# Performance work log

Measured on AMD Instinct MI355X. Metric: run time of the kernel, lower is better.

The kernel has to match this reference:

```python
import jax, jax.numpy as jnp
import numpy as np

D = 384
H = 6
DK = D // H
EPS = 1e-5


def _layernorm(x, g, b):
    mu = jnp.mean(x, axis=-1, keepdims=True)
    var = jnp.var(x, axis=-1, keepdims=True)
    return (x - mu) * jax.lax.rsqrt(var + EPS) * g + b


def setup_inputs() -> dict:
    key = jax.random.key(0)
    ks = jax.random.split(key, 12)
    B, N = 8, 2048
    s = lambda fan_in: 1.0 / np.sqrt(fan_in)
    return {
        "points": jax.random.normal(ks[0], (B, 3 + D, N), dtype=jnp.float32),
        "ln1_g": jnp.ones((D,), jnp.float32),
        "ln1_b": jnp.zeros((D,), jnp.float32),
        "w_qkv": jax.random.uniform(ks[1], (3 * D, D), jnp.float32, -s(D), s(D)),
        "w_o": jax.random.uniform(ks[2], (D, D), jnp.float32, -s(D), s(D)),
        "b_o": jnp.zeros((D,), jnp.float32),
        "ln2_g": jnp.ones((D,), jnp.float32),
        "ln2_b": jnp.zeros((D,), jnp.float32),
        "w1": jax.random.uniform(ks[3], (2 * D, D), jnp.float32, -s(D), s(D)),
        "b1": jnp.zeros((2 * D,), jnp.float32),
        "w2": jax.random.uniform(ks[4], (D, 2 * D), jnp.float32, -s(2 * D), s(2 * D)),
        "b2": jnp.zeros((D,), jnp.float32),
    }


def reference(points, ln1_g, ln1_b, w_qkv, w_o, b_o, ln2_g, ln2_b, w1, b1, w2, b2):
    coords = points[:, :3, :]                       # [B, 3, N]
    feats = jnp.transpose(points[:, 3:, :], (0, 2, 1))  # [B, N, D]
    B, N, _ = feats.shape

    # pre-norm + fused QKV projection (no bias)
    h = _layernorm(feats, ln1_g, ln1_b)
    qkv = jnp.einsum('bnd,ed->bne', h, w_qkv)       # [B, N, 3D]
    q, k, v = jnp.split(qkv, 3, axis=-1)

    split_heads = lambda t: jnp.transpose(t.reshape(B, N, H, DK), (0, 2, 1, 3))
    q, k, v = split_heads(q), split_heads(k), split_heads(v)  # [B, H, N, DK]

    scale = DK ** -0.5
    scores = jnp.einsum('bhid,bhjd->bhij', q, k) * scale      # [B, H, N, N]
    attn = jax.nn.softmax(scores, axis=-1)
    ctx = jnp.einsum('bhij,bhjd->bhid', attn, v)              # [B, H, N, DK]
    ctx = jnp.transpose(ctx, (0, 2, 1, 3)).reshape(B, N, D)
    attn_out = jnp.einsum('bnd,ed->bne', ctx, w_o) + b_o

    x = feats + attn_out
    # FFN with exact (erf) GELU, hidden = 2*D
    h2 = _layernorm(x, ln2_g, ln2_b)
    ff = jnp.einsum('bnd,ed->bne', h2, w1) + b1
    ff = jax.nn.gelu(ff, approximate=False)
    ff = jnp.einsum('bne,de->bnd', ff, w2) + b2
    x = x + ff

    return jnp.concatenate([coords, jnp.transpose(x, (0, 2, 1))], axis=1)
```

## Files before the change

kernel.cpp:

```cpp
#include <hip/hip_runtime.h>
#include <cstdint>


typedef __bf16 bf16;
typedef __bf16 bf16x8 __attribute__((ext_vector_type(8)));
typedef __bf16 bf16x4 __attribute__((ext_vector_type(4)));
typedef short s16x4 __attribute__((ext_vector_type(4)));
typedef float floatx4 __attribute__((ext_vector_type(4)));
typedef uint32_t __attribute__((address_space(1))) gu32;
typedef uint32_t __attribute__((address_space(3))) lu32;

#define NN 2048
#define DD 384
#define HH 6
#define DK 64
#define BB 8
#define MM (BB * NN)
#define D3 (3 * DD)
#define D2 (2 * DD)
#define CH (3 + DD)
#define LP 72
#define LPV 136

#define QSCALE 0.18033688011112042f

static __device__ __forceinline__ s16x4 as_s16x4(bf16x4 v) {
    union { bf16x4 b; s16x4 s; } u; u.b = v; return u.s;
}


__global__ void cast_all_kernel(const float* __restrict__ w_qkv, const float* __restrict__ w_o,
                                const float* __restrict__ w1, const float* __restrict__ w2,
                                bf16* __restrict__ o_qkv, bf16* __restrict__ o_o,
                                bf16* __restrict__ o_w1, bf16* __restrict__ o_w2) {
    int i = blockIdx.x * 256 + threadIdx.x;
    if (i < 442368) o_qkv[i] = (bf16)w_qkv[i];
    else if (i < 589824) o_o[i - 442368] = (bf16)w_o[i - 442368];
    else if (i < 884736) o_w1[i - 589824] = (bf16)w1[i - 589824];
    else o_w2[i - 884736] = (bf16)w2[i - 884736];
}

__global__ void coords_kernel(const float* __restrict__ pts, float* __restrict__ out) {
    int i = blockIdx.x * 256 + threadIdx.x;
    int b = i / (3 * NN), r = i % (3 * NN);
    out[(size_t)b * CH * NN + r] = pts[(size_t)b * CH * NN + r];
}

__global__ void transpose_kernel(const float* __restrict__ pts, float* __restrict__ feats) {
    __shared__ float T[32][33];
    int n0 = blockIdx.x * 32, d0 = blockIdx.y * 32, b = blockIdx.z;
    int tx = threadIdx.x, ty = threadIdx.y;
    const float* src = pts + (size_t)b * CH * NN;
#pragma unroll
    for (int i = 0; i < 4; ++i)
        T[ty + i * 8][tx] = src[(size_t)(3 + d0 + ty + i * 8) * NN + n0 + tx];
    __syncthreads();
    float* dst = feats + (size_t)b * NN * DD;
#pragma unroll
    for (int i = 0; i < 4; ++i)
        dst[(size_t)(n0 + ty + i * 8) * DD + d0 + tx] = T[tx][ty + i * 8];
}

__global__ __launch_bounds__(256) void ln_kernel(const float* __restrict__ x,
                                                 const float* __restrict__ g,
                                                 const float* __restrict__ bta,
                                                 bf16* __restrict__ out) {
    int wave = threadIdx.x >> 6, lane = threadIdx.x & 63;
    int row = blockIdx.x * 4 + wave;
    const float* xr = x + (size_t)row * DD;
    float v[6], s = 0.f, sq = 0.f;
#pragma unroll
    for (int i = 0; i < 6; ++i) { v[i] = xr[lane + i * 64]; s += v[i]; sq += v[i] * v[i]; }
#pragma unroll
    for (int o = 1; o < 64; o <<= 1) { s += __shfl_xor(s, o); sq += __shfl_xor(sq, o); }
    float mu = s * (1.f / DD);
    float var = sq * (1.f / DD) - mu * mu;
    float rs = rsqrtf(var + 1e-5f);
    bf16* orow = out + (size_t)row * DD;
#pragma unroll
    for (int i = 0; i < 6; ++i) {
        int d = lane + i * 64;
        orow[d] = (bf16)((v[i] - mu) * rs * g[d] + bta[d]);
    }
}

template <int NC, int K, int MODE, int TN>
__global__ __launch_bounds__(256, 2)
void gemm_bt(const bf16* __restrict__ A, const bf16* __restrict__ W,
             const float* __restrict__ bias, const float* __restrict__ res,
             bf16* __restrict__ obf, float* __restrict__ of32, bf16* __restrict__ vt) {
    constexpr int MI = (TN == 128) ? 4 : 2;
    __shared__ bf16 As[128 * 32];
    __shared__ bf16 Ws[TN * 32];
    const int t = threadIdx.x;
    const int wave = t >> 6, lane = t & 63;
    const int m0 = blockIdx.x * 128, n0 = blockIdx.y * TN;
    const int wm = (TN == 128) ? (wave >> 1) * 64 : wave * 32;
    const int wn = (TN == 128) ? (wave & 1) * 64 : 0;
    const int lr = lane & 15, quad = lane >> 4;
    const int sr = t >> 2, sc = (t & 3) * 8;

    floatx4 acc[MI][4];
#pragma unroll
    for (int mi = 0; mi < MI; ++mi)
#pragma unroll
        for (int ni = 0; ni < 4; ++ni) {
            floatx4 z = {0.f, 0.f, 0.f, 0.f};
            acc[mi][ni] = z;
        }

    for (int k0 = 0; k0 < K; k0 += 32) {
        __syncthreads();
#pragma unroll
        for (int i = 0; i < 2; ++i) {
            const int r = i * 64 + sr;
            __builtin_amdgcn_global_load_lds(
                (const gu32*)&A[(size_t)(m0 + r) * K + k0 + sc],
                (lu32*)&As[r * 32 + sc], 16, 0, 0);
        }
#pragma unroll
        for (int i = 0; i < TN / 64; ++i) {
            const int r = i * 64 + sr;
            __builtin_amdgcn_global_load_lds(
                (const gu32*)&W[(size_t)(n0 + r) * K + k0 + sc],
                (lu32*)&Ws[r * 32 + sc], 16, 0, 0);
        }
        __syncthreads();
        bf16x8 af[MI], bfr[4];
#pragma unroll
        for (int mi = 0; mi < MI; ++mi)
            af[mi] = *(const bf16x8*)&As[(wm + mi * 16 + lr) * 32 + quad * 8];
#pragma unroll
        for (int ni = 0; ni < 4; ++ni)
            bfr[ni] = *(const bf16x8*)&Ws[(wn + ni * 16 + lr) * 32 + quad * 8];
#pragma unroll
        for (int mi = 0; mi < MI; ++mi)
#pragma unroll
            for (int ni = 0; ni < 4; ++ni)
                acc[mi][ni] = __builtin_amdgcn_mfma_f32_16x16x32_bf16(af[mi], bfr[ni], acc[mi][ni], 0, 0, 0);
    }

#pragma unroll
    for (int mi = 0; mi < MI; ++mi) {
#pragma unroll
        for (int ni = 0; ni < 4; ++ni) {
            const int r0 = m0 + wm + mi * 16 + quad * 4;
            const int c = n0 + wn + ni * 16 + lr;
            floatx4 v = acc[mi][ni];
            if constexpr (MODE == 0) {
                const int cb = n0 + wn + ni * 16;
                if (cb >= 2 * DD) {
                    const int hh = (c - 2 * DD) >> 6, dk = (c - 2 * DD) & 63;
                    const int b = r0 >> 11, n = r0 & (NN - 1);
                    bf16x4 pk;
#pragma unroll
                    for (int r = 0; r < 4; ++r) pk[r] = (bf16)v[r];
                    *(bf16x4*)&vt[((size_t)(b * HH + hh) * DK + dk) * NN + n] = pk;
                } else {
                    const float sc_q = (cb < DD) ? QSCALE : 1.0f;
#pragma unroll
                    for (int r = 0; r < 4; ++r) obf[(size_t)(r0 + r) * NC + c] = (bf16)(v[r] * sc_q);
                }
            } else if constexpr (MODE == 1) {
#pragma unroll
                for (int r = 0; r < 4; ++r)
                    of32[(size_t)(r0 + r) * NC + c] = v[r] + bias[c] + res[(size_t)(r0 + r) * NC + c];
            } else if constexpr (MODE == 2) {
#pragma unroll
                for (int r = 0; r < 4; ++r) {
                    float u = v[r] + bias[c];
                    obf[(size_t)(r0 + r) * NC + c] = (bf16)(0.5f * u * (1.f + erff(u * 0.70710678118f)));
                }
            } else {
                const int b = r0 >> 11, n = r0 & (NN - 1);
                float o4[4];
#pragma unroll
                for (int r = 0; r < 4; ++r)
                    o4[r] = v[r] + bias[c] + res[(size_t)(r0 + r) * DD + c];
                float4 val = make_float4(o4[0], o4[1], o4[2], o4[3]);
                *(float4*)&of32[((size_t)b * CH + 3 + c) * NN + n] = val;
            }
        }
    }
}

__global__ __launch_bounds__(256, 3)
void attn_kernel(const bf16* __restrict__ qkv, const bf16* __restrict__ vt,
                 bf16* __restrict__ ctx) {
    __shared__ bf16 Ks[128 * LP];
    __shared__ bf16 Vs[64 * LPV];
    const int t = threadIdx.x, wave = t >> 6, lane = t & 63;
    const int lr = lane & 15, quad = lane >> 4;
    const int bh = blockIdx.y, b = bh / HH, h = bh % HH;
    const int q0 = blockIdx.x * 128 + wave * 32;
    const bf16* qbase = qkv + (size_t)b * NN * D3 + h * DK;
    const bf16* kbase = qbase + DD;
    const bf16* vbase = vt + (size_t)bh * DK * NN;

    bf16x8 aq[2][2];
#pragma unroll
    for (int mi = 0; mi < 2; ++mi)
#pragma unroll
        for (int ks = 0; ks < 2; ++ks)
            aq[mi][ks] = *(const bf16x8*)&qbase[(size_t)(q0 + mi * 16 + lr) * D3 +
                                                ks * 32 + quad * 8];

    bf16x4 ones4;
#pragma unroll
    for (int i = 0; i < 4; ++i) ones4[i] = (bf16)1.0f;
    const s16x4 ones_s = as_s16x4(ones4);

    floatx4 o[2][4], ol[2];
#pragma unroll
    for (int mi = 0; mi < 2; ++mi) {
        floatx4 z = {0.f, 0.f, 0.f, 0.f};
        ol[mi] = z;
#pragma unroll
        for (int nd = 0; nd < 4; ++nd) o[mi][nd] = z;
    }

    for (int j0 = 0; j0 < NN; j0 += 128) {
        __syncthreads();
        {
            const int rr = t >> 3, cc = (t & 7) * 8;
#pragma unroll
            for (int i = 0; i < 4; ++i) {
                const int j = i * 32 + rr;
                *(bf16x8*)&Ks[j * LP + cc] =
                    *(const bf16x8*)&kbase[(size_t)(j0 + j) * D3 + cc];
            }
            const int rr2 = t >> 4, cc2 = (t & 15) * 8;
#pragma unroll
            for (int i = 0; i < 4; ++i) {
                const int d = i * 16 + rr2;
                *(bf16x8*)&Vs[d * LPV + cc2] =
                    *(const bf16x8*)&vbase[(size_t)d * NN + j0 + cc2];
            }
        }
        __syncthreads();

        floatx4 s[2][8];
#pragma unroll
        for (int mi = 0; mi < 2; ++mi)
#pragma unroll
            for (int nj = 0; nj < 8; ++nj) {
                floatx4 z = {0.f, 0.f, 0.f, 0.f};
                s[mi][nj] = z;
            }
#pragma unroll
        for (int ks = 0; ks < 2; ++ks)
#pragma unroll
            for (int nj = 0; nj < 8; ++nj) {
                bf16x8 bk = *(const bf16x8*)&Ks[(nj * 16 + lr) * LP + ks * 32 + quad * 8];
#pragma unroll
                for (int mi = 0; mi < 2; ++mi)
                    s[mi][nj] = __builtin_amdgcn_mfma_f32_16x16x32_bf16(bk, aq[mi][ks],
                                                                        s[mi][nj], 0, 0, 0);
            }

#pragma unroll
        for (int nj = 0; nj < 8; ++nj) {
            s16x4 ap[2];
#pragma unroll
            for (int mi = 0; mi < 2; ++mi) {
                bf16x4 pk;
#pragma unroll
                for (int r = 0; r < 4; ++r) pk[r] = (bf16)exp2f(s[mi][nj][r]);
                ap[mi] = as_s16x4(pk);
            }
#pragma unroll
            for (int nd = 0; nd < 4; ++nd) {
                s16x4 bv = as_s16x4(*(const bf16x4*)&Vs[(nd * 16 + lr) * LPV +
                                                        nj * 16 + quad * 4]);
#pragma unroll
                for (int mi = 0; mi < 2; ++mi)
                    o[mi][nd] = __builtin_amdgcn_mfma_f32_16x16x16bf16_1k(ap[mi], bv,
                                                                          o[mi][nd], 0, 0, 0);
            }
#pragma unroll
            for (int mi = 0; mi < 2; ++mi)
                ol[mi] = __builtin_amdgcn_mfma_f32_16x16x16bf16_1k(ap[mi], ones_s, ol[mi], 0, 0, 0);
        }
    }

#pragma unroll
    for (int mi = 0; mi < 2; ++mi)
#pragma unroll
        for (int r = 0; r < 4; ++r) {
            const int n = q0 + mi * 16 + quad * 4 + r;
            const float inv = 1.0f / ol[mi][r];
#pragma unroll
            for (int nd = 0; nd < 4; ++nd) {
                const int d = h * DK + nd * 16 + lr;
                ctx[(size_t)(b * NN + n) * DD + d] = (bf16)(o[mi][nd][r] * inv);
            }
        }
}


extern "C" void kernel_launch(void* const* d_in, const int* in_sizes, int n_in,
                              void* d_out, int out_size, void* d_ws, size_t ws_size,
                              hipStream_t stream) {
    const float* points = (const float*)d_in[0];
    const float* ln1_g = (const float*)d_in[1];
    const float* ln1_b = (const float*)d_in[2];
    const float* w_qkv = (const float*)d_in[3];
    const float* w_o   = (const float*)d_in[4];
    const float* b_o   = (const float*)d_in[5];
    const float* ln2_g = (const float*)d_in[6];
    const float* ln2_b = (const float*)d_in[7];
    const float* w1    = (const float*)d_in[8];
    const float* b1    = (const float*)d_in[9];
    const float* w2    = (const float*)d_in[10];
    const float* b2    = (const float*)d_in[11];
    float* out = (float*)d_out;

    char* ws = (char*)d_ws;
    size_t off = 0;
    auto alloc = [&](size_t bytes) -> void* {
        void* p = ws + off;
        off += (bytes + 255) & ~(size_t)255;
        return p;
    };
    float* feats = (float*)alloc((size_t)MM * DD * 4);
    float* xbuf  = (float*)alloc((size_t)MM * DD * 4);
    bf16* h1     = (bf16*)alloc((size_t)MM * DD * 2);
    bf16* h2     = (bf16*)alloc((size_t)MM * DD * 2);
    bf16* qkvb   = (bf16*)alloc((size_t)MM * D3 * 2);
    bf16* vtb    = (bf16*)alloc((size_t)BB * HH * DK * NN * 2);
    bf16* ctx    = (bf16*)alloc((size_t)MM * DD * 2);
    bf16* ffh    = (bf16*)alloc((size_t)MM * D2 * 2);
    bf16* wqkv_bf = (bf16*)alloc((size_t)D3 * DD * 2);
    bf16* wo_bf   = (bf16*)alloc((size_t)DD * DD * 2);
    bf16* w1_bf   = (bf16*)alloc((size_t)D2 * DD * 2);
    bf16* w2_bf   = (bf16*)alloc((size_t)DD * D2 * 2);

    cast_all_kernel<<<1179648 / 256, 256, 0, stream>>>(w_qkv, w_o, w1, w2,
                                                       wqkv_bf, wo_bf, w1_bf, w2_bf);
    coords_kernel<<<(BB * 3 * NN) / 256, 256, 0, stream>>>(points, out);
    transpose_kernel<<<dim3(NN / 32, DD / 32, BB), dim3(32, 8), 0, stream>>>(points, feats);
    ln_kernel<<<MM / 4, 256, 0, stream>>>(feats, ln1_g, ln1_b, h1);
    gemm_bt<D3, DD, 0, 128><<<dim3(MM / 128, D3 / 128), 256, 0, stream>>>(
        h1, wqkv_bf, nullptr, nullptr, qkvb, nullptr, vtb);
    attn_kernel<<<dim3(NN / 128, BB * HH), 256, 0, stream>>>(qkvb, vtb, ctx);
    gemm_bt<DD, DD, 1, 64><<<dim3(MM / 128, DD / 64), 256, 0, stream>>>(
        ctx, wo_bf, b_o, feats, nullptr, xbuf, nullptr);
    ln_kernel<<<MM / 4, 256, 0, stream>>>(xbuf, ln2_g, ln2_b, h2);
    gemm_bt<D2, DD, 2, 128><<<dim3(MM / 128, D2 / 128), 256, 0, stream>>>(
        h2, w1_bf, b1, nullptr, ffh, nullptr, nullptr);
    gemm_bt<DD, D2, 3, 64><<<dim3(MM / 128, DD / 64), 256, 0, stream>>>(
        ffh, w2_bf, b2, xbuf, nullptr, out, nullptr);
}
```

Before: 290.5 us.

## Prefetch next K/V tile into registers and raise wave priority around MFMA blocks

The attention kernel now loads the next 128-key K and V tiles from global memory into registers while the current tile is being computed, then writes them to shared memory at the top of the next iteration. This hides global load latency behind the QK and PV MFMA work. It also wraps the MFMA sections in s_setprio so waves issuing matrix ops get scheduling priority. The cost is 8 extra vector registers per thread, which may pressure occupancy at launch bounds of 3 blocks.

```diff
diff --git a/kernel.cpp b/kernel.cpp
--- a/kernel.cpp
+++ b/kernel.cpp
@@ -197,6 +197,9 @@
     const bf16* kbase = qbase + DD;
     const bf16* vbase = vt + (size_t)bh * DK * NN;
 
+    const int rr = t >> 3, cc = (t & 7) * 8;
+    const int rr2 = t >> 4, cc2 = (t & 15) * 8;
+
     bf16x8 aq[2][2];
 #pragma unroll
     for (int mi = 0; mi < 2; ++mi)
@@ -219,23 +222,30 @@
         for (int nd = 0; nd < 4; ++nd) o[mi][nd] = z;
     }
 
+    bf16x8 pk[4], pv[4];
+#pragma unroll
+    for (int i = 0; i < 4; ++i)
+        pk[i] = *(const bf16x8*)&kbase[(size_t)(i * 32 + rr) * D3 + cc];
+#pragma unroll
+    for (int i = 0; i < 4; ++i)
+        pv[i] = *(const bf16x8*)&vbase[(size_t)(i * 16 + rr2) * NN + cc2];
+
     for (int j0 = 0; j0 < NN; j0 += 128) {
         __syncthreads();
-        {
-            const int rr = t >> 3, cc = (t & 7) * 8;
-#pragma unroll
-            for (int i = 0; i < 4; ++i) {
-                const int j = i * 32 + rr;
-                *(bf16x8*)&Ks[j * LP + cc] =
-                    *(const bf16x8*)&kbase[(size_t)(j0 + j) * D3 + cc];
-            }
-            const int rr2 = t >> 4, cc2 = (t & 15) * 8;
-#pragma unroll
-            for (int i = 0; i < 4; ++i) {
-                const int d = i * 16 + rr2;
-                *(bf16x8*)&Vs[d * LPV + cc2] =
-                    *(const bf16x8*)&vbase[(size_t)d * NN + j0 + cc2];
-            }
+#pragma unroll
+        for (int i = 0; i < 4; ++i)
+            *(bf16x8*)&Ks[(i * 32 + rr) * LP + cc] = pk[i];
+#pragma unroll
+        for (int i = 0; i < 4; ++i)
+            *(bf16x8*)&Vs[(i * 16 + rr2) * LPV + cc2] = pv[i];
+        if (j0 + 128 < NN) {
+            const int jn = j0 + 128;
+#pragma unroll
+            for (int i = 0; i < 4; ++i)
+                pk[i] = *(const bf16x8*)&kbase[(size_t)(jn + i * 32 + rr) * D3 + cc];
+#pragma unroll
+            for (int i = 0; i < 4; ++i)
+                pv[i] = *(const bf16x8*)&vbase[(size_t)(i * 16 + rr2) * NN + jn + cc2];
         }
         __syncthreads();
 
@@ -247,6 +257,7 @@
                 floatx4 z = {0.f, 0.f, 0.f, 0.f};
                 s[mi][nj] = z;
             }
+        __builtin_amdgcn_s_setprio(1);
 #pragma unroll
         for (int ks = 0; ks < 2; ++ks)
 #pragma unroll
@@ -257,17 +268,19 @@
                     s[mi][nj] = __builtin_amdgcn_mfma_f32_16x16x32_bf16(bk, aq[mi][ks],
                                                                         s[mi][nj], 0, 0, 0);
             }
+        __builtin_amdgcn_s_setprio(0);
 
 #pragma unroll
         for (int nj = 0; nj < 8; ++nj) {
             s16x4 ap[2];
 #pragma unroll
             for (int mi = 0; mi < 2; ++mi) {
-                bf16x4 pk;
-#pragma unroll
-                for (int r = 0; r < 4; ++r) pk[r] = (bf16)exp2f(s[mi][nj][r]);
-                ap[mi] = as_s16x4(pk);
-            }
+                bf16x4 pk4;
+#pragma unroll
+                for (int r = 0; r < 4; ++r) pk4[r] = (bf16)exp2f(s[mi][nj][r]);
+                ap[mi] = as_s16x4(pk4);
+            }
+            __builtin_amdgcn_s_setprio(1);
 #pragma unroll
             for (int nd = 0; nd < 4; ++nd) {
                 s16x4 bv = as_s16x4(*(const bf16x4*)&Vs[(nd * 16 + lr) * LPV +
@@ -280,6 +293,7 @@
 #pragma unroll
             for (int mi = 0; mi < 2; ++mi)
                 ol[mi] = __builtin_amdgcn_mfma_f32_16x16x16bf16_1k(ap[mi], ones_s, ol[mi], 0, 0, 0);
+            __builtin_amdgcn_s_setprio(0);
         }
     }
 
```

New measurement: 334.6 us. 15.2% more time.
